# Performance work log

Hardware: AMD Instinct MI355X
Metric: run time of the kernel (lower is better)

Reference implementation:

```python
import jax, jax.numpy as jnp
import numpy as np

B, S, D, H = 2, 2048, 1024, 16
DK = D // H
NEG = -1e9


def setup_inputs() -> dict:
    key = jax.random.key(0)
    ks = jax.random.split(key, 12)
    inp = {
        "query": jax.random.normal(ks[0], (B, S, D), jnp.float32),
        "key": jax.random.normal(ks[1], (B, S, D), jnp.float32),
        "value": jax.random.normal(ks[2], (B, S, D), jnp.float32),
        "mask": jax.random.randint(ks[3], (B, S), 0, 2, jnp.int32),
    }
    # 4 linears (q, k, v, out), each d_model x d_model with bias.
    scale = 1.0 / np.sqrt(D)
    for i, name in enumerate(["wq", "wk", "wv", "wo"]):
        inp[name] = jax.random.uniform(ks[4 + i], (D, D), jnp.float32, -scale, scale)
        inp["b" + name[1]] = jax.random.uniform(ks[8 + i], (D,), jnp.float32, -scale, scale)
    return inp


def _split_heads(x):  # [B,S,D] -> [B,H,S,DK]
    return x.reshape(B, S, H, DK).transpose(0, 2, 1, 3)


def reference(query, key, value, mask, wq, bq, wk, bk, wv, bv, wo, bo):
    q = _split_heads(query @ wq.T + bq)
    k = _split_heads(key @ wk.T + bk)
    v = _split_heads(value @ wv.T + bv)
    scores = jnp.einsum("bhqd,bhkd->bhqk", q, k) / jnp.sqrt(jnp.float32(DK))
    # mask: [B,S] -> [B,1,1,S]; masked_fill where mask == 0
    m = mask[:, None, None, :]
    scores = jnp.where(m == 0, NEG, scores)
    attn = jax.nn.softmax(scores, axis=-1)  # dropout p=0 (eval) -> identity
    x = jnp.einsum("bhqk,bhkd->bhqd", attn, v)
    x = x.transpose(0, 2, 1, 3).reshape(B, S, D)
    return x @ wo.T + bo
```

## Files before the change

### kernel.cpp

```cpp
#include <hip/hip_runtime.h>


typedef _Float16 f16;
typedef _Float16 f16x8 __attribute__((ext_vector_type(8)));
typedef _Float16 f16x4 __attribute__((ext_vector_type(4)));
typedef __fp16 fp16x2r __attribute__((ext_vector_type(2)));
typedef float f32x4 __attribute__((ext_vector_type(4)));

union F16x4u { f16x4 v; fp16x2r h[2]; };

#define MFMA_F16(a, b, c) __builtin_amdgcn_mfma_f32_16x16x32_f16((a), (b), (c), 0, 0, 0)
#define L2E 1.44269504088896340736f

__device__ __forceinline__ void gld16(const void* g, void* l) {
    __builtin_amdgcn_global_load_lds(
        (__attribute__((address_space(1))) void*)(g),
        (__attribute__((address_space(3))) void*)(l), 16, 0, 0);
}

__global__ __launch_bounds__(256) void cvt_kernel(
    const float* __restrict__ q, const float* __restrict__ k,
    const float* __restrict__ v,
    const float* __restrict__ wq, const float* __restrict__ wk,
    const float* __restrict__ wv, const float* __restrict__ wo,
    f16* __restrict__ oq, f16* __restrict__ ok, f16* __restrict__ ov,
    f16* __restrict__ owq, f16* __restrict__ owk, f16* __restrict__ owv,
    f16* __restrict__ owo)
{
    const int z = blockIdx.y;
    const float* src;
    f16* dst;
    int n;
    switch (z) {
        case 0: src = q;  dst = oq;  n = 4194304; break;
        case 1: src = k;  dst = ok;  n = 4194304; break;
        case 2: src = v;  dst = ov;  n = 4194304; break;
        case 3: src = wq; dst = owq; n = 1048576; break;
        case 4: src = wk; dst = owk; n = 1048576; break;
        case 5: src = wv; dst = owv; n = 1048576; break;
        default: src = wo; dst = owo; n = 1048576; break;
    }
    int idx = (blockIdx.x * 256 + threadIdx.x) * 8;
    if (idx >= n) return;
    float4 a = *(const float4*)(src + idx);
    float4 b = *(const float4*)(src + idx + 4);
    f16x8 h = { (f16)a.x, (f16)a.y, (f16)a.z, (f16)a.w,
                (f16)b.x, (f16)b.y, (f16)b.z, (f16)b.w };
    *(f16x8*)(dst + idx) = h;
}

__global__ __launch_bounds__(256) void proj_qkv_kernel(
    const f16* __restrict__ xq, const f16* __restrict__ xk,
    const f16* __restrict__ xv,
    const f16* __restrict__ wqh, const f16* __restrict__ wkh,
    const f16* __restrict__ wvh,
    const float* __restrict__ bq, const float* __restrict__ bk,
    const float* __restrict__ bv,
    f16* __restrict__ qh, f16* __restrict__ kh, f16* __restrict__ vt)
{
    const int z = blockIdx.z;
    const f16* X = (z == 0) ? xq : (z == 1) ? xk : xv;
    const f16* W = (z == 0) ? wqh : (z == 1) ? wkh : wvh;
    const float* bias = (z == 0) ? bq : (z == 1) ? bk : bv;
    const f16* P0 = (z < 2) ? W : X;
    const f16* P1 = (z < 2) ? X : W;

    __shared__ __align__(16) f16 smem[16384];
    f16* As = smem;
    f16* Bs = smem + 8192;
    f16* L  = smem;

    const int t = threadIdx.x;
    const int wave = t >> 6, lane = t & 63, quad = lane >> 4, l15 = lane & 15;
    const int m_base = (wave >> 1) * 64, n_base = (wave & 1) * 64;
    const int blockM = (z < 2) ? blockIdx.y * 128 : blockIdx.x * 128;
    const int blockN = (z < 2) ? blockIdx.x * 128 : blockIdx.y * 128;

    const int srow = lane >> 3;
    const int sblk = (lane & 7) ^ srow;

    f32x4 acc[4][4];
#pragma unroll
    for (int mt = 0; mt < 4; mt++)
#pragma unroll
        for (int nt = 0; nt < 4; nt++)
            acc[mt][nt] = (f32x4){0.f, 0.f, 0.f, 0.f};

    for (int k0 = 0; k0 < 1024; k0 += 64) {
        __syncthreads();
#pragma unroll
        for (int j = 0; j < 4; j++) {
            int r0 = wave * 32 + j * 8;
            gld16(&P0[(size_t)(blockM + r0 + srow) * 1024 + k0 + sblk * 8],
                  &As[r0 * 64]);
            gld16(&P1[(size_t)(blockN + r0 + srow) * 1024 + k0 + sblk * 8],
                  &Bs[r0 * 64]);
        }
        __syncthreads();

#pragma unroll
        for (int c = 0; c < 2; c++) {
            f16x8 af[4], bf[4];
#pragma unroll
            for (int mt = 0; mt < 4; mt++)
                af[mt] = *(const f16x8*)(&As[(m_base + mt * 16 + l15) * 64 +
                                             (((c * 4 + quad) ^ (l15 & 7)) << 3)]);
#pragma unroll
            for (int nt = 0; nt < 4; nt++)
                bf[nt] = *(const f16x8*)(&Bs[(n_base + nt * 16 + l15) * 64 +
                                             (((c * 4 + quad) ^ (l15 & 7)) << 3)]);
#pragma unroll
            for (int mt = 0; mt < 4; mt++)
#pragma unroll
                for (int nt = 0; nt < 4; nt++)
                    acc[mt][nt] = MFMA_F16(af[mt], bf[nt], acc[mt][nt]);
        }
    }

    if (z < 2) {
        f16* o = (z == 0) ? qh : kh;
        const float scale = (z == 0) ? 0.125f * L2E : 1.0f;
        float4 b4[4];
#pragma unroll
        for (int mt = 0; mt < 4; mt++)
            b4[mt] = *(const float4*)(&bias[blockM + m_base + mt * 16 + quad * 4]);

#pragma unroll
        for (int half = 0; half < 2; half++) {
            __syncthreads();
            if ((wave & 1) == half) {
#pragma unroll
                for (int mt = 0; mt < 4; mt++)
#pragma unroll
                    for (int nt = 0; nt < 4; nt++) {
                        f16x4 pk = {
                            (f16)((acc[mt][nt][0] + b4[mt].x) * scale),
                            (f16)((acc[mt][nt][1] + b4[mt].y) * scale),
                            (f16)((acc[mt][nt][2] + b4[mt].z) * scale),
                            (f16)((acc[mt][nt][3] + b4[mt].w) * scale) };
                        *(f16x4*)(&L[(nt * 16 + l15) * 136 +
                                     m_base + mt * 16 + quad * 4]) = pk;
                    }
            }
            __syncthreads();
#pragma unroll
            for (int pass = 0; pass < 4; pass++) {
                int unit = pass * 32 + (t >> 3);
                int hh = unit >> 6, s_loc = unit & 63;
                f16x8 vv = *(const f16x8*)(&L[s_loc * 136 + hh * 64 + (t & 7) * 8]);
                int s_glob = blockN + half * 64 + s_loc;
                int b = s_glob >> 11, s = s_glob & 2047;
                int h_glob = (blockM >> 6) + hh;
                *(f16x8*)(&o[(((size_t)(b * 16 + h_glob) * 2048 + s) << 6) +
                             (t & 7) * 8]) = vv;
            }
        }
    } else {
        float bv_[4];
#pragma unroll
        for (int nt = 0; nt < 4; nt++)
            bv_[nt] = bias[blockN + n_base + nt * 16 + l15];

#pragma unroll
        for (int half = 0; half < 2; half++) {
            __syncthreads();
            if ((wave & 1) == half) {
#pragma unroll
                for (int mt = 0; mt < 4; mt++)
#pragma unroll
                    for (int nt = 0; nt < 4; nt++) {
                        f16x4 pk = { (f16)(acc[mt][nt][0] + bv_[nt]),
                                     (f16)(acc[mt][nt][1] + bv_[nt]),
                                     (f16)(acc[mt][nt][2] + bv_[nt]),
                                     (f16)(acc[mt][nt][3] + bv_[nt]) };
                        *(f16x4*)(&L[(nt * 16 + l15) * 136 +
                                     m_base + mt * 16 + quad * 4]) = pk;
                    }
            }
            __syncthreads();
#pragma unroll
            for (int pass = 0; pass < 4; pass++) {
                int f_loc = pass * 16 + (t >> 4);
                f16x8 vv = *(const f16x8*)(&L[f_loc * 136 + (t & 15) * 8]);
                int feat = blockN + half * 64 + f_loc;
                int hh = feat >> 6, dk = feat & 63;
                int b = blockM >> 11;
                int s0 = (blockM & 2047) + (t & 15) * 8;
                *(f16x8*)(&vt[((size_t)((b * 16 + hh) * 64 + dk) << 11) + s0]) = vv;
            }
        }
    }
}

__device__ __forceinline__ void flash_stage2(
    const f16* kbase, const f16* vbase, int key0,
    f16* Kb, f16* Vb, int wg, int srow8, int sblk)
{
#pragma unroll
    for (int p = 0; p < 2; p++) {
        int r0 = wg * 16 + p * 8;
        int row = r0 + srow8;
        gld16(&kbase[(size_t)(key0 + row) * 64 + sblk * 8], &Kb[r0 * 64]);
        gld16(&vbase[(size_t)row * 2048 + key0 + sblk * 8], &Vb[r0 * 64]);
    }
}

__device__ __forceinline__ void flash_phase2(
    const f16* Kbuf, const f16* Vbuf, const float* bias_all, int key0,
    const f16x8 (&qf)[2][2], int quad, int l15,
    f32x4 (&O)[2][4], f32x4 (&lacc)[2])
{
    f32x4 sc[2][4];
#pragma unroll
    for (int nt = 0; nt < 4; nt++) {
        const f16* krow = &Kbuf[(nt * 16 + l15) * 64];
        f16x8 kf0 = *(const f16x8*)(&krow[(quad ^ (l15 & 7)) << 3]);
        f16x8 kf1 = *(const f16x8*)(&krow[((quad + 4) ^ (l15 & 7)) << 3]);
        float4 b4 = *(const float4*)(&bias_all[key0 + nt * 16 + quad * 4]);
#pragma unroll
        for (int cb = 0; cb < 2; cb++) {
            f32x4 z4 = (f32x4){b4.x, b4.y, b4.z, b4.w};
            z4 = MFMA_F16(kf0, qf[cb][0], z4);
            sc[cb][nt] = MFMA_F16(kf1, qf[cb][1], z4);
        }
    }
    const f16x8 ones8 = {(f16)1.f, (f16)1.f, (f16)1.f, (f16)1.f,
                         (f16)1.f, (f16)1.f, (f16)1.f, (f16)1.f};
    union P8 { f16x8 v8; f16x4 v4[2]; };
    P8 pp[2][2];
#pragma unroll
    for (int cb = 0; cb < 2; cb++) {
#pragma unroll
        for (int nt = 0; nt < 4; nt++) {
            float p0 = exp2f(sc[cb][nt][0]);
            float p1 = exp2f(sc[cb][nt][1]);
            float p2 = exp2f(sc[cb][nt][2]);
            float p3 = exp2f(sc[cb][nt][3]);
            F16x4u u;
            u.h[0] = __builtin_amdgcn_cvt_pkrtz(p0, p1);
            u.h[1] = __builtin_amdgcn_cvt_pkrtz(p2, p3);
            pp[cb][nt >> 1].v4[nt & 1] = u.v;
        }
        lacc[cb] = MFMA_F16(ones8, pp[cb][0].v8, lacc[cb]);
        lacc[cb] = MFMA_F16(ones8, pp[cb][1].v8, lacc[cb]);
    }
#pragma unroll
    for (int nto = 0; nto < 4; nto++) {
        const f16* vrow = &Vbuf[(nto * 16 + l15) * 64];
        P8 va, vb;
        va.v4[0] = *(const f16x4*)(&vrow[(((quad >> 1) ^ (l15 & 7)) << 3) + (quad & 1) * 4]);
        va.v4[1] = *(const f16x4*)(&vrow[(((2 + (quad >> 1)) ^ (l15 & 7)) << 3) + (quad & 1) * 4]);
        vb.v4[0] = *(const f16x4*)(&vrow[(((4 + (quad >> 1)) ^ (l15 & 7)) << 3) + (quad & 1) * 4]);
        vb.v4[1] = *(const f16x4*)(&vrow[(((6 + (quad >> 1)) ^ (l15 & 7)) << 3) + (quad & 1) * 4]);
#pragma unroll
        for (int cb = 0; cb < 2; cb++) {
            O[cb][nto] = MFMA_F16(va.v8, pp[cb][0].v8, O[cb][nto]);
            O[cb][nto] = MFMA_F16(vb.v8, pp[cb][1].v8, O[cb][nto]);
        }
    }
}

__global__ __launch_bounds__(512, 4) void flash_kernel(
    const f16* __restrict__ qh, const f16* __restrict__ kh,
    const f16* __restrict__ vt, const int* __restrict__ mask,
    f16* __restrict__ ctx)
{
    __shared__ __align__(16) f16 KV[8 * 4096];
    __shared__ float bias_all[2048];

    const int t = threadIdx.x;
    const int wave = t >> 6, lane = t & 63, quad = lane >> 4, l15 = lane & 15;
    const int group = wave >> 2, wg = wave & 3;
    const int bh = blockIdx.x;
    const int b = bh >> 4, h = bh & 15;
    const int q0 = blockIdx.y * 128;

    const f16* qbase = qh + (size_t)bh * (2048 * 64);
    const f16* kbase = kh + (size_t)bh * (2048 * 64);
    const f16* vbase = vt + (size_t)bh * (64 * 2048);

    f16* K0 = &KV[((0 * 2 + group) * 2 + 0) * 4096];
    f16* V0 = &KV[((0 * 2 + group) * 2 + 1) * 4096];
    f16* K1 = &KV[((1 * 2 + group) * 2 + 0) * 4096];
    f16* V1 = &KV[((1 * 2 + group) * 2 + 1) * 4096];

#pragma unroll
    for (int j = 0; j < 4; j++) {
        int i = j * 512 + t;
        bias_all[i] = (mask[b * 2048 + i] == 0) ? -1.0e9f : 0.0f;
    }

    f16x8 qf[2][2];
#pragma unroll
    for (int cb = 0; cb < 2; cb++) {
        int qrow = q0 + wg * 32 + cb * 16 + l15;
        qf[cb][0] = *(const f16x8*)(&qbase[qrow * 64 + quad * 8]);
        qf[cb][1] = *(const f16x8*)(&qbase[qrow * 64 + 32 + quad * 8]);
    }

    f32x4 O[2][4];
#pragma unroll
    for (int cb = 0; cb < 2; cb++)
#pragma unroll
        for (int n = 0; n < 4; n++) O[cb][n] = (f32x4){0.f, 0.f, 0.f, 0.f};
    f32x4 lacc[2] = {(f32x4){0.f, 0.f, 0.f, 0.f}, (f32x4){0.f, 0.f, 0.f, 0.f}};

    const int srow8 = lane >> 3;
    const int sblk = (lane & 7) ^ srow8;

    flash_stage2(kbase, vbase, group * 64, K0, V0, wg, srow8, sblk);

    for (int k2 = 0; k2 < 16; k2 += 2) {
        __syncthreads();
        flash_stage2(kbase, vbase, (k2 + 1) * 128 + group * 64, K1, V1,
                     wg, srow8, sblk);
        flash_phase2(K0, V0, bias_all, k2 * 128 + group * 64,
                     qf, quad, l15, O, lacc);
        __syncthreads();
        if (k2 < 14)
            flash_stage2(kbase, vbase, (k2 + 2) * 128 + group * 64, K0, V0,
                         wg, srow8, sblk);
        flash_phase2(K1, V1, bias_all, (k2 + 1) * 128 + group * 64,
                     qf, quad, l15, O, lacc);
    }

    __syncthreads();
    float* Red = (float*)KV;
    const int t4 = wg * 64 + lane;
    if (group == 1) {
#pragma unroll
        for (int cb = 0; cb < 2; cb++) {
#pragma unroll
            for (int nto = 0; nto < 4; nto++)
                *(f32x4*)(&Red[(cb * 4 + nto) * 1024 + t4 * 4]) = O[cb][nto];
            Red[8 * 1024 + cb * 256 + t4] = lacc[cb][0];
        }
    }
    __syncthreads();
    if (group == 0) {
#pragma unroll
        for (int cb = 0; cb < 2; cb++) {
            const float l2 = Red[8 * 1024 + cb * 256 + t4];
            const float inv_l = 1.0f / (lacc[cb][0] + l2);
            int qrow = q0 + wg * 32 + cb * 16 + l15;
#pragma unroll
            for (int nto = 0; nto < 4; nto++) {
                f32x4 o2 = *(const f32x4*)(&Red[(cb * 4 + nto) * 1024 + t4 * 4]);
                f16x4 pk = { (f16)((O[cb][nto][0] + o2[0]) * inv_l),
                             (f16)((O[cb][nto][1] + o2[1]) * inv_l),
                             (f16)((O[cb][nto][2] + o2[2]) * inv_l),
                             (f16)((O[cb][nto][3] + o2[3]) * inv_l) };
                *(f16x4*)(&ctx[(size_t)(b * 2048 + qrow) * 1024 + h * 64 +
                               nto * 16 + quad * 4]) = pk;
            }
        }
    }
}

__global__ __launch_bounds__(256) void proj_out_kernel(
    const f16* __restrict__ ctx, const f16* __restrict__ woh,
    const float* __restrict__ bo, float* __restrict__ out)
{
    __shared__ __align__(16) f16 As[2][128 * 64];
    __shared__ __align__(16) f16 Bs[2][64 * 64];

    const int t = threadIdx.x;
    const int wave = t >> 6, lane = t & 63, quad = lane >> 4, l15 = lane & 15;
    const int m_base = (wave >> 1) * 64, n_base = (wave & 1) * 32;
    const int blockM = blockIdx.x * 128;
    const int blockN = blockIdx.y * 64;

    const int srow = lane >> 3;
    const int sblk = (lane & 7) ^ srow;

    f32x4 acc[4][2];
#pragma unroll
    for (int mt = 0; mt < 4; mt++)
#pragma unroll
        for (int nt = 0; nt < 2; nt++)
            acc[mt][nt] = (f32x4){0.f, 0.f, 0.f, 0.f};

#pragma unroll
    for (int j = 0; j < 4; j++) {
        int r0 = wave * 32 + j * 8;
        gld16(&ctx[(size_t)(blockM + r0 + srow) * 1024 + sblk * 8],
              &As[0][r0 * 64]);
    }
#pragma unroll
    for (int j = 0; j < 2; j++) {
        int r0 = wave * 16 + j * 8;
        gld16(&woh[(size_t)(blockN + r0 + srow) * 1024 + sblk * 8],
              &Bs[0][r0 * 64]);
    }

    for (int ki = 0; ki < 16; ki++) {
        const int cur = ki & 1;
        __syncthreads();

        if (ki < 15) {
            const int k0n = (ki + 1) * 64;
#pragma unroll
            for (int j = 0; j < 4; j++) {
                int r0 = wave * 32 + j * 8;
                gld16(&ctx[(size_t)(blockM + r0 + srow) * 1024 + k0n + sblk * 8],
                      &As[cur ^ 1][r0 * 64]);
            }
#pragma unroll
            for (int j = 0; j < 2; j++) {
                int r0 = wave * 16 + j * 8;
                gld16(&woh[(size_t)(blockN + r0 + srow) * 1024 + k0n + sblk * 8],
                      &Bs[cur ^ 1][r0 * 64]);
            }
        }

#pragma unroll
        for (int c = 0; c < 2; c++) {
            f16x8 af[4], bf[2];
#pragma unroll
            for (int mt = 0; mt < 4; mt++)
                af[mt] = *(const f16x8*)(&As[cur][(m_base + mt * 16 + l15) * 64 +
                                              (((c * 4 + quad) ^ (l15 & 7)) << 3)]);
#pragma unroll
            for (int nt = 0; nt < 2; nt++)
                bf[nt] = *(const f16x8*)(&Bs[cur][(n_base + nt * 16 + l15) * 64 +
                                              (((c * 4 + quad) ^ (l15 & 7)) << 3)]);
#pragma unroll
            for (int mt = 0; mt < 4; mt++)
#pragma unroll
                for (int nt = 0; nt < 2; nt++)
                    acc[mt][nt] = MFMA_F16(af[mt], bf[nt], acc[mt][nt]);
        }
    }

    float bo_[2];
#pragma unroll
    for (int nt = 0; nt < 2; nt++)
        bo_[nt] = bo[blockN + n_base + nt * 16 + l15];

#pragma unroll
    for (int mt = 0; mt < 4; mt++) {
        int row0 = blockM + m_base + mt * 16 + quad * 4;
#pragma unroll
        for (int nt = 0; nt < 2; nt++) {
            int col_g = blockN + n_base + nt * 16 + l15;
#pragma unroll
            for (int i = 0; i < 4; i++)
                out[(size_t)(row0 + i) * 1024 + col_g] = acc[mt][nt][i] + bo_[nt];
        }
    }
}

extern "C" void kernel_launch(void* const* d_in, const int* in_sizes, int n_in,
                              void* d_out, int out_size, void* d_ws, size_t ws_size,
                              hipStream_t stream) {
    const float* query = (const float*)d_in[0];
    const float* key_  = (const float*)d_in[1];
    const float* value = (const float*)d_in[2];
    const int*   mask  = (const int*)d_in[3];
    const float* wq = (const float*)d_in[4];
    const float* bq = (const float*)d_in[5];
    const float* wk = (const float*)d_in[6];
    const float* bk = (const float*)d_in[7];
    const float* wv = (const float*)d_in[8];
    const float* bv = (const float*)d_in[9];
    const float* wo = (const float*)d_in[10];
    const float* bo = (const float*)d_in[11];
    float* out = (float*)d_out;

    f16* xq  = (f16*)d_ws;
    f16* xk  = xq  + 4194304;
    f16* xv  = xk  + 4194304;
    f16* wqh = xv  + 4194304;
    f16* wkh = wqh + 1048576;
    f16* wvh = wkh + 1048576;
    f16* woh = wvh + 1048576;
    f16* qh  = woh + 1048576;
    f16* kh  = qh  + 4194304;
    f16* vt  = kh  + 4194304;
    f16* ctx = xq;

    cvt_kernel<<<dim3(2048, 7), 256, 0, stream>>>(
        query, key_, value, wq, wk, wv, wo, xq, xk, xv, wqh, wkh, wvh, woh);
    proj_qkv_kernel<<<dim3(32, 8, 3), 256, 0, stream>>>(
        xq, xk, xv, wqh, wkh, wvh, bq, bk, bv, qh, kh, vt);
    flash_kernel<<<dim3(32, 16), 512, 0, stream>>>(qh, kh, vt, mask, ctx);
    proj_out_kernel<<<dim3(32, 16), 256, 0, stream>>>(ctx, woh, bo, out);
}
```

Measured before the change: 230.4 us.

## Pre-permute V^T layout so flash kernel loads V fragments with 128-bit reads

The V-transpose epilogue now writes V^T with keys permuted inside each 64-key block. This lets the flash kernel's PV stage read each V fragment with a single 16-byte LDS load instead of four 8-byte loads. It also switches exp2f to the raw hardware exp2 builtin and replaces the launch bounds with explicit flat-work-group-size and waves-per-EU attributes. The permutation has to match the P fragment ordering exactly, so correctness depends on the producer and consumer layouts agreeing.

```diff
diff --git a/kernel.cpp b/kernel.cpp
--- a/kernel.cpp
+++ b/kernel.cpp
@@ -6,8 +6,6 @@
 typedef _Float16 f16x4 __attribute__((ext_vector_type(4)));
 typedef __fp16 fp16x2r __attribute__((ext_vector_type(2)));
 typedef float f32x4 __attribute__((ext_vector_type(4)));
-
-union F16x4u { f16x4 v; fp16x2r h[2]; };
 
 #define MFMA_F16(a, b, c) __builtin_amdgcn_mfma_f32_16x16x32_f16((a), (b), (c), 0, 0, 0)
 #define L2E 1.44269504088896340736f
@@ -181,11 +179,20 @@
 #pragma unroll
             for (int pass = 0; pass < 4; pass++) {
                 int f_loc = pass * 16 + (t >> 4);
-                f16x8 vv = *(const f16x8*)(&L[f_loc * 136 + (t & 15) * 8]);
+                int tt = t & 15;
+                int bb = (tt >= 8) ? 64 : 0;
+                int o  = (tt & 7) * 8;
+                int p  = (o >> 5) & 1;
+                int c  = (o >> 3) & 3;
+                int g1 = bb + p * 32 + c * 4;
+                const f16* Lrow = &L[f_loc * 136];
+                f16x4 lo = *(const f16x4*)(&Lrow[g1]);
+                f16x4 hi = *(const f16x4*)(&Lrow[g1 + 16]);
+                f16x8 vv = __builtin_shufflevector(lo, hi, 0, 1, 2, 3, 4, 5, 6, 7);
                 int feat = blockN + half * 64 + f_loc;
                 int hh = feat >> 6, dk = feat & 63;
                 int b = blockM >> 11;
-                int s0 = (blockM & 2047) + (t & 15) * 8;
+                int s0 = (blockM & 2047) + bb + o;
                 *(f16x8*)(&vt[((size_t)((b * 16 + hh) * 64 + dk) << 11) + s0]) = vv;
             }
         }
@@ -210,12 +217,13 @@
     const f16x8 (&qf)[2][2], int quad, int l15,
     f32x4 (&O)[2][4], f32x4 (&lacc)[2])
 {
+    const int sw = l15 & 7;
     f32x4 sc[2][4];
 #pragma unroll
     for (int nt = 0; nt < 4; nt++) {
         const f16* krow = &Kbuf[(nt * 16 + l15) * 64];
-        f16x8 kf0 = *(const f16x8*)(&krow[(quad ^ (l15 & 7)) << 3]);
-        f16x8 kf1 = *(const f16x8*)(&krow[((quad + 4) ^ (l15 & 7)) << 3]);
+        f16x8 kf0 = *(const f16x8*)(&krow[(quad ^ sw) << 3]);
+        f16x8 kf1 = *(const f16x8*)(&krow[((quad + 4) ^ sw) << 3]);
         float4 b4 = *(const float4*)(&bias_all[key0 + nt * 16 + quad * 4]);
 #pragma unroll
         for (int cb = 0; cb < 2; cb++) {
@@ -226,20 +234,18 @@
     }
     const f16x8 ones8 = {(f16)1.f, (f16)1.f, (f16)1.f, (f16)1.f,
                          (f16)1.f, (f16)1.f, (f16)1.f, (f16)1.f};
-    union P8 { f16x8 v8; f16x4 v4[2]; };
-    P8 pp[2][2];
+    union P8u { f16x8 v8; fp16x2r h[4]; };
+    P8u pp[2][2];
 #pragma unroll
     for (int cb = 0; cb < 2; cb++) {
 #pragma unroll
         for (int nt = 0; nt < 4; nt++) {
-            float p0 = exp2f(sc[cb][nt][0]);
-            float p1 = exp2f(sc[cb][nt][1]);
-            float p2 = exp2f(sc[cb][nt][2]);
-            float p3 = exp2f(sc[cb][nt][3]);
-            F16x4u u;
-            u.h[0] = __builtin_amdgcn_cvt_pkrtz(p0, p1);
-            u.h[1] = __builtin_amdgcn_cvt_pkrtz(p2, p3);
-            pp[cb][nt >> 1].v4[nt & 1] = u.v;
+            float p0 = __builtin_amdgcn_exp2f(sc[cb][nt][0]);
+            float p1 = __builtin_amdgcn_exp2f(sc[cb][nt][1]);
+            float p2 = __builtin_amdgcn_exp2f(sc[cb][nt][2]);
+            float p3 = __builtin_amdgcn_exp2f(sc[cb][nt][3]);
+            pp[cb][nt >> 1].h[(nt & 1) * 2 + 0] = __builtin_amdgcn_cvt_pkrtz(p0, p1);
+            pp[cb][nt >> 1].h[(nt & 1) * 2 + 1] = __builtin_amdgcn_cvt_pkrtz(p2, p3);
         }
         lacc[cb] = MFMA_F16(ones8, pp[cb][0].v8, lacc[cb]);
         lacc[cb] = MFMA_F16(ones8, pp[cb][1].v8, lacc[cb]);
@@ -247,20 +253,20 @@
 #pragma unroll
     for (int nto = 0; nto < 4; nto++) {
         const f16* vrow = &Vbuf[(nto * 16 + l15) * 64];
-        P8 va, vb;
-        va.v4[0] = *(const f16x4*)(&vrow[(((quad >> 1) ^ (l15 & 7)) << 3) + (quad & 1) * 4]);
-        va.v4[1] = *(const f16x4*)(&vrow[(((2 + (quad >> 1)) ^ (l15 & 7)) << 3) + (quad & 1) * 4]);
-        vb.v4[0] = *(const f16x4*)(&vrow[(((4 + (quad >> 1)) ^ (l15 & 7)) << 3) + (quad & 1) * 4]);
-        vb.v4[1] = *(const f16x4*)(&vrow[(((6 + (quad >> 1)) ^ (l15 & 7)) << 3) + (quad & 1) * 4]);
+        f16x8 va = *(const f16x8*)(&vrow[(quad ^ sw) << 3]);
+        f16x8 vb = *(const f16x8*)(&vrow[((4 + quad) ^ sw) << 3]);
 #pragma unroll
         for (int cb = 0; cb < 2; cb++) {
-            O[cb][nto] = MFMA_F16(va.v8, pp[cb][0].v8, O[cb][nto]);
-            O[cb][nto] = MFMA_F16(vb.v8, pp[cb][1].v8, O[cb][nto]);
-        }
-    }
-}
-
-__global__ __launch_bounds__(512, 4) void flash_kernel(
+            O[cb][nto] = MFMA_F16(va, pp[cb][0].v8, O[cb][nto]);
+            O[cb][nto] = MFMA_F16(vb, pp[cb][1].v8, O[cb][nto]);
+        }
+    }
+}
+
+__global__
+__attribute__((amdgpu_flat_work_group_size(512, 512)))
+__attribute__((amdgpu_waves_per_eu(4, 4)))
+void flash_kernel(
     const f16* __restrict__ qh, const f16* __restrict__ kh,
     const f16* __restrict__ vt, const int* __restrict__ mask,
     f16* __restrict__ ctx)
```

Measured after the change: 212.7 us. 1.08x faster.
